# Optimization experiments

Hardware: AMD Instinct MI355X
Metric: run time of the kernel (lower is better)

The kernel has to match this reference:

```python
import jax, jax.numpy as jnp
import numpy as np

B, S, H, O, N, R = 16, 1024, 4096, 4096, 8, 64  # batch, seq, in, out, n_adapters, rank
P_DROP = 0.1


def setup_inputs() -> dict:
    key = jax.random.key(0)
    ks = jax.random.split(key, 6)
    result = jax.random.normal(ks[0], (B, S, O), dtype=jnp.float32)  # base-layer output (residual)
    data = jax.random.normal(ks[1], (B, S, H), dtype=jnp.float32)    # hidden states
    keep = 1.0 - P_DROP
    # inverted-dropout mask: values in {0, 1/keep}, reproduces F.dropout(train) exactly
    mask = jax.random.bernoulli(ks[2], keep, (B, S, H)).astype(jnp.float32) / keep
    lora_a = jax.random.normal(ks[3], (N, R, H), dtype=jnp.float32) * 0.02  # per-adapter A
    lora_b = jax.random.normal(ks[4], (N, O, R), dtype=jnp.float32) * 0.02  # per-adapter B
    scalings = jax.random.uniform(ks[5], (N,), dtype=jnp.float32, minval=0.25, maxval=2.0)  # alpha/r per adapter
    return {"result": result, "data": data, "mask": mask,
            "lora_a": lora_a, "lora_b": lora_b, "scalings": scalings}


def reference(result, data, mask, lora_a, lora_b, scalings):
    # Multi-adapter batched LoRA: batch is partitioned into N equal segments,
    # each owned by one adapter. Equivalent to LoraFunction.forward's loop:
    #   drop = dropout(data[s:e]) * scaling; result[s:e] += (drop @ A^T) @ B^T
    per = B // N  # sequences per adapter segment
    x = (data * mask).reshape(N, per, S, H) * scalings[:, None, None, None]
    t = jnp.einsum('npsh,nrh->npsr', x, lora_a)        # [N, per, S, R]
    delta = jnp.einsum('npsr,nor->npso', t, lora_b)    # [N, per, S, O]
    return result + delta.reshape(B, S, O)
```

## Files before the change

### kernel.cpp

```cpp
#include <hip/hip_runtime.h>


#define B_   16
#define S_   1024
#define H_   4096
#define O_   4096
#define N_   8
#define R_   64
#define ROWS (B_ * S_)
#define ROWS_PER_ADAPTER (ROWS / N_)

typedef __attribute__((ext_vector_type(8))) short s8v;
typedef __attribute__((ext_vector_type(4))) float f4v;

static __device__ __forceinline__ short f2bf(float f) {
    union { float f; unsigned u; } v; v.f = f;
    unsigned r = (v.u + 0x7FFFu + ((v.u >> 16) & 1u)) >> 16;
    return (short)r;
}

__global__ void cvt_weights(const float* __restrict__ la,
                            const float* __restrict__ lb,
                            const float* __restrict__ scal,
                            short* __restrict__ abf,
                            short* __restrict__ bbf) {
    const int i = blockIdx.x * blockDim.x + threadIdx.x;
    const int A_ELEMS4 = (N_ * R_ * H_) / 4;
    if (i < A_ELEMS4) {
        const int n = i / ((R_ * H_) / 4);
        const float s = scal[n];
        float4 v = ((const float4*)la)[i];
        short4 o;
        o.x = f2bf(v.x * s); o.y = f2bf(v.y * s);
        o.z = f2bf(v.z * s); o.w = f2bf(v.w * s);
        ((short4*)abf)[i] = o;
    } else {
        const int j = i - A_ELEMS4;
        float4 v = ((const float4*)lb)[j];
        short4 o;
        o.x = f2bf(v.x); o.y = f2bf(v.y);
        o.z = f2bf(v.z); o.w = f2bf(v.w);
        ((short4*)bbf)[j] = o;
    }
}

__global__ __launch_bounds__(512, 4)
void lora_fused(const float* __restrict__ data, const float* __restrict__ mask,
                const short* __restrict__ abf, const short* __restrict__ bbf,
                const float* __restrict__ result, float* __restrict__ out) {
    __shared__ float part[8][16][66];
    __shared__ short tl[16][80];

    const int tile = blockIdx.x;
    const int row0 = tile * 16;
    const int n    = row0 / ROWS_PER_ADAPTER;
    const int tid  = threadIdx.x;
    const int w    = tid >> 6;
    const int lane = tid & 63;
    const int ml   = lane & 15;
    const int g    = lane >> 4;

    const int row = row0 + ml;
    const int k0  = w * 512 + g * 8;
    const float* dptr = data + (size_t)row * H_ + k0;
    const float* mptr = mask + (size_t)row * H_ + k0;
    const short* ap0 = abf + (size_t)(n * R_ +  0 + ml) * H_ + k0;
    const short* ap1 = abf + (size_t)(n * R_ + 16 + ml) * H_ + k0;
    const short* ap2 = abf + (size_t)(n * R_ + 32 + ml) * H_ + k0;
    const short* ap3 = abf + (size_t)(n * R_ + 48 + ml) * H_ + k0;

    f4v acc0 = {0.f, 0.f, 0.f, 0.f};
    f4v acc1 = {0.f, 0.f, 0.f, 0.f};
    f4v acc2 = {0.f, 0.f, 0.f, 0.f};
    f4v acc3 = {0.f, 0.f, 0.f, 0.f};

#pragma unroll 2
    for (int ks = 0; ks < 512 / 32; ++ks) {
        float4 d0 = *(const float4*)(dptr);
        float4 d1 = *(const float4*)(dptr + 4);
        float4 m0 = *(const float4*)(mptr);
        float4 m1 = *(const float4*)(mptr + 4);
        s8v a0 = *(const s8v*)(ap0);
        s8v a1 = *(const s8v*)(ap1);
        s8v a2 = *(const s8v*)(ap2);
        s8v a3 = *(const s8v*)(ap3);

        s8v xf;
        xf[0] = f2bf(d0.x * m0.x); xf[1] = f2bf(d0.y * m0.y);
        xf[2] = f2bf(d0.z * m0.z); xf[3] = f2bf(d0.w * m0.w);
        xf[4] = f2bf(d1.x * m1.x); xf[5] = f2bf(d1.y * m1.y);
        xf[6] = f2bf(d1.z * m1.z); xf[7] = f2bf(d1.w * m1.w);

        acc0 = __builtin_amdgcn_mfma_f32_16x16x32_bf16(xf, a0, acc0, 0, 0, 0);
        acc1 = __builtin_amdgcn_mfma_f32_16x16x32_bf16(xf, a1, acc1, 0, 0, 0);
        acc2 = __builtin_amdgcn_mfma_f32_16x16x32_bf16(xf, a2, acc2, 0, 0, 0);
        acc3 = __builtin_amdgcn_mfma_f32_16x16x32_bf16(xf, a3, acc3, 0, 0, 0);

        dptr += 32; mptr += 32;
        ap0 += 32; ap1 += 32; ap2 += 32; ap3 += 32;
    }

#pragma unroll
    for (int i = 0; i < 4; ++i) {
        part[w][g * 4 + i][ 0 + ml] = acc0[i];
        part[w][g * 4 + i][16 + ml] = acc1[i];
        part[w][g * 4 + i][32 + ml] = acc2[i];
        part[w][g * 4 + i][48 + ml] = acc3[i];
    }
    __syncthreads();

    {
        const int e0 = tid * 2;
        const int rw = e0 >> 6;
        const int c  = e0 & 63;
        float s0 = 0.f, s1 = 0.f;
#pragma unroll
        for (int p = 0; p < 8; ++p) {
            float2 v = *(const float2*)&part[p][rw][c];
            s0 += v.x; s1 += v.y;
        }
        tl[rw][c]     = f2bf(s0);
        tl[rw][c + 1] = f2bf(s1);
    }
    __syncthreads();

    s8v tf0 = *(const s8v*)&tl[ml][g * 8];
    s8v tf1 = *(const s8v*)&tl[ml][g * 8 + 32];

    const short* bptr = bbf + ((size_t)n * O_ + w * 512 + ml) * R_ + g * 8;
    const size_t obase0 = (size_t)(row0 + g * 4) * O_ + w * 512 + ml;

#pragma unroll 2
    for (int ot = 0; ot < 32; ++ot) {
        s8v bf0 = *(const s8v*)(bptr);
        s8v bf1 = *(const s8v*)(bptr + 32);
        f4v acc = {0.f, 0.f, 0.f, 0.f};
        acc = __builtin_amdgcn_mfma_f32_16x16x32_bf16(tf0, bf0, acc, 0, 0, 0);
        acc = __builtin_amdgcn_mfma_f32_16x16x32_bf16(tf1, bf1, acc, 0, 0, 0);

        const size_t base = obase0 + (size_t)ot * 16;
#pragma unroll
        for (int i = 0; i < 4; ++i) {
            out[base + (size_t)i * O_] = result[base + (size_t)i * O_] + acc[i];
        }
        bptr += 16 * R_;
    }
}

extern "C" void kernel_launch(void* const* d_in, const int* in_sizes, int n_in,
                              void* d_out, int out_size, void* d_ws, size_t ws_size,
                              hipStream_t stream) {
    const float* result = (const float*)d_in[0];
    const float* data   = (const float*)d_in[1];
    const float* mask   = (const float*)d_in[2];
    const float* lora_a = (const float*)d_in[3];
    const float* lora_b = (const float*)d_in[4];
    const float* scal   = (const float*)d_in[5];
    float* out = (float*)d_out;

    short* abf = (short*)d_ws;
    short* bbf = abf + (size_t)N_ * R_ * H_;

    const int cvt_threads = (N_ * R_ * H_ + N_ * O_ * R_) / 4;
    cvt_weights<<<cvt_threads / 256, 256, 0, stream>>>(lora_a, lora_b, scal, abf, bbf);
    lora_fused<<<dim3(ROWS / 16), 512, 0, stream>>>(data, mask, abf, bbf, result, out);
}
```

Baseline: 826.2 us.

## Software-prefetch both GEMM loops and vectorize output stores via transposed MFMA

Both MFMA loops now use register double-buffering: the next iteration's data, mask, A, B and result loads are issued before the current iteration's compute, hiding global memory latency. The second GEMM swaps its MFMA operands so each lane holds four consecutive output columns of one row. This lets result reads and output writes be single float4 accesses instead of four strided scalar ones. Register pressure rises under the 512x4 launch bounds, which could cause spills or lower occupancy.

```diff
diff --git a/kernel.cpp b/kernel.cpp
--- a/kernel.cpp
+++ b/kernel.cpp
@@ -74,16 +74,26 @@
     f4v acc2 = {0.f, 0.f, 0.f, 0.f};
     f4v acc3 = {0.f, 0.f, 0.f, 0.f};
 
-#pragma unroll 2
-    for (int ks = 0; ks < 512 / 32; ++ks) {
-        float4 d0 = *(const float4*)(dptr);
-        float4 d1 = *(const float4*)(dptr + 4);
-        float4 m0 = *(const float4*)(mptr);
-        float4 m1 = *(const float4*)(mptr + 4);
-        s8v a0 = *(const s8v*)(ap0);
-        s8v a1 = *(const s8v*)(ap1);
-        s8v a2 = *(const s8v*)(ap2);
-        s8v a3 = *(const s8v*)(ap3);
+    float4 d0 = *(const float4*)(dptr);
+    float4 d1 = *(const float4*)(dptr + 4);
+    float4 m0 = *(const float4*)(mptr);
+    float4 m1 = *(const float4*)(mptr + 4);
+    s8v a0 = *(const s8v*)(ap0);
+    s8v a1 = *(const s8v*)(ap1);
+    s8v a2 = *(const s8v*)(ap2);
+    s8v a3 = *(const s8v*)(ap3);
+
+    for (int ks = 0; ks < 15; ++ks) {
+        dptr += 32; mptr += 32;
+        ap0 += 32; ap1 += 32; ap2 += 32; ap3 += 32;
+        float4 nd0 = *(const float4*)(dptr);
+        float4 nd1 = *(const float4*)(dptr + 4);
+        float4 nm0 = *(const float4*)(mptr);
+        float4 nm1 = *(const float4*)(mptr + 4);
+        s8v na0 = *(const s8v*)(ap0);
+        s8v na1 = *(const s8v*)(ap1);
+        s8v na2 = *(const s8v*)(ap2);
+        s8v na3 = *(const s8v*)(ap3);
 
         s8v xf;
         xf[0] = f2bf(d0.x * m0.x); xf[1] = f2bf(d0.y * m0.y);
@@ -96,8 +106,19 @@
         acc2 = __builtin_amdgcn_mfma_f32_16x16x32_bf16(xf, a2, acc2, 0, 0, 0);
         acc3 = __builtin_amdgcn_mfma_f32_16x16x32_bf16(xf, a3, acc3, 0, 0, 0);
 
-        dptr += 32; mptr += 32;
-        ap0 += 32; ap1 += 32; ap2 += 32; ap3 += 32;
+        d0 = nd0; d1 = nd1; m0 = nm0; m1 = nm1;
+        a0 = na0; a1 = na1; a2 = na2; a3 = na3;
+    }
+    {
+        s8v xf;
+        xf[0] = f2bf(d0.x * m0.x); xf[1] = f2bf(d0.y * m0.y);
+        xf[2] = f2bf(d0.z * m0.z); xf[3] = f2bf(d0.w * m0.w);
+        xf[4] = f2bf(d1.x * m1.x); xf[5] = f2bf(d1.y * m1.y);
+        xf[6] = f2bf(d1.z * m1.z); xf[7] = f2bf(d1.w * m1.w);
+        acc0 = __builtin_amdgcn_mfma_f32_16x16x32_bf16(xf, a0, acc0, 0, 0, 0);
+        acc1 = __builtin_amdgcn_mfma_f32_16x16x32_bf16(xf, a1, acc1, 0, 0, 0);
+        acc2 = __builtin_amdgcn_mfma_f32_16x16x32_bf16(xf, a2, acc2, 0, 0, 0);
+        acc3 = __builtin_amdgcn_mfma_f32_16x16x32_bf16(xf, a3, acc3, 0, 0, 0);
     }
 
 #pragma unroll
@@ -128,22 +149,38 @@
     s8v tf1 = *(const s8v*)&tl[ml][g * 8 + 32];
 
     const short* bptr = bbf + ((size_t)n * O_ + w * 512 + ml) * R_ + g * 8;
-    const size_t obase0 = (size_t)(row0 + g * 4) * O_ + w * 512 + ml;
-
-#pragma unroll 2
-    for (int ot = 0; ot < 32; ++ot) {
-        s8v bf0 = *(const s8v*)(bptr);
-        s8v bf1 = *(const s8v*)(bptr + 32);
+    const float* rrow = result + (size_t)(row0 + ml) * O_ + w * 512 + g * 4;
+    float*       orow = out    + (size_t)(row0 + ml) * O_ + w * 512 + g * 4;
+
+    s8v bf0 = *(const s8v*)(bptr);
+    s8v bf1 = *(const s8v*)(bptr + 32);
+    float4 rv = *(const float4*)(rrow);
+
+    for (int ot = 0; ot < 31; ++ot) {
+        bptr += 16 * R_;
+        s8v nbf0 = *(const s8v*)(bptr);
+        s8v nbf1 = *(const s8v*)(bptr + 32);
+        float4 nrv = *(const float4*)(rrow + (ot + 1) * 16);
+
         f4v acc = {0.f, 0.f, 0.f, 0.f};
-        acc = __builtin_amdgcn_mfma_f32_16x16x32_bf16(tf0, bf0, acc, 0, 0, 0);
-        acc = __builtin_amdgcn_mfma_f32_16x16x32_bf16(tf1, bf1, acc, 0, 0, 0);
-
-        const size_t base = obase0 + (size_t)ot * 16;
-#pragma unroll
-        for (int i = 0; i < 4; ++i) {
-            out[base + (size_t)i * O_] = result[base + (size_t)i * O_] + acc[i];
-        }
-        bptr += 16 * R_;
+        acc = __builtin_amdgcn_mfma_f32_16x16x32_bf16(bf0, tf0, acc, 0, 0, 0);
+        acc = __builtin_amdgcn_mfma_f32_16x16x32_bf16(bf1, tf1, acc, 0, 0, 0);
+
+        float4 ov;
+        ov.x = rv.x + acc[0]; ov.y = rv.y + acc[1];
+        ov.z = rv.z + acc[2]; ov.w = rv.w + acc[3];
+        *(float4*)(orow + ot * 16) = ov;
+
+        bf0 = nbf0; bf1 = nbf1; rv = nrv;
+    }
+    {
+        f4v acc = {0.f, 0.f, 0.f, 0.f};
+        acc = __builtin_amdgcn_mfma_f32_16x16x32_bf16(bf0, tf0, acc, 0, 0, 0);
+        acc = __builtin_amdgcn_mfma_f32_16x16x32_bf16(bf1, tf1, acc, 0, 0, 0);
+        float4 ov;
+        ov.x = rv.x + acc[0]; ov.y = rv.y + acc[1];
+        ov.z = rv.z + acc[2]; ov.w = rv.w + acc[3];
+        *(float4*)(orow + 31 * 16) = ov;
     }
 }
 
```

Result: no change. 840.6 us (+1.7%).
